# Kernel optimization log

Hardware: AMD Instinct MI355X
Metric: run time of the kernel (lower is better)

The kernel has to match this reference:

```python
import jax, jax.numpy as jnp
import numpy as np

N = 8192          # num nodes
E = 262144        # num edges
F_IN = 512        # dataset.num_features
HID = 256         # hidden_dim
C = 16            # dataset.num_classes
ALPHA = 1.0
GAMMA = 1.0
EPS = 0.4
LN_EPS = 1e-5


def setup_inputs() -> dict:
    key = jax.random.key(0)
    ks = jax.random.split(key, 16)
    x = jax.random.normal(ks[0], (N, F_IN), dtype=jnp.float32)
    edge_index = jax.random.randint(ks[1], (2, E), 0, N, dtype=jnp.int64)
    def lin(k, fan_in, fan_out):
        s = 1.0 / np.sqrt(fan_in)
        return jax.random.uniform(k, (fan_in, fan_out), jnp.float32, -s, s)
    return {
        "x": x,
        "edge_index": edge_index,
        "W0": lin(ks[2], F_IN, HID), "b0": jnp.zeros((HID,), jnp.float32),
        "ln0_g": jnp.ones((HID,), jnp.float32), "ln0_b": jnp.zeros((HID,), jnp.float32),
        "W1": lin(ks[3], HID, HID), "b1": jnp.zeros((HID,), jnp.float32),
        "ln1_g": jnp.ones((HID,), jnp.float32), "ln1_b": jnp.zeros((HID,), jnp.float32),
        "W2": lin(ks[4], HID, C), "b2": jnp.zeros((C,), jnp.float32),
    }


def _layernorm(h, g, b):
    mu = jnp.mean(h, axis=-1, keepdims=True)
    var = jnp.var(h, axis=-1, keepdims=True)
    return (h - mu) * jax.lax.rsqrt(var + LN_EPS) * g + b


def _hpf_weight_matrix(edge_index, n, dtype):
    # to_dense_adj with parallel-edge accumulation
    A = jnp.zeros((n, n), dtype).at[edge_index[0], edge_index[1]].add(jnp.asarray(1.0, dtype))
    eye = jnp.eye(n, dtype=dtype)
    A = GAMMA * A + ALPHA * eye
    # D^{-1/2} A D^{-1/2} as fused row/col scaling (same math as the two diag matmuls)
    dinv = jax.lax.rsqrt(jnp.sum(A, axis=1))
    A_hat = dinv[:, None] * A * dinv[None, :]
    # (eps - 1) I + (I - A_hat) == eps*I - A_hat ; keep only positive entries (edge extraction)
    U = EPS * eye - A_hat
    return jnp.where(U > 0, U, jnp.asarray(0.0, dtype))


def reference(x, edge_index, W0, b0, ln0_g, ln0_b, W1, b1, ln1_g, ln1_b, W2, b2):
    Wmat = _hpf_weight_matrix(edge_index, x.shape[0], x.dtype)
    # GCNConv(normalize=False): h' = scatter_{src->tgt}(w * (h@W)[src]) + bias == Wmat^T @ (h@W) + b
    def gcn(h, W, b):
        return Wmat.T @ (h @ W) + b
    h = gcn(x, W0, b0)
    h = _layernorm(jax.nn.relu(h), ln0_g, ln0_b)   # dropout p=0.0 -> identity
    h = gcn(h, W1, b1)
    h = _layernorm(jax.nn.relu(h), ln1_g, ln1_b)
    embedding = gcn(h, W2, b2)
    return embedding, jax.nn.log_softmax(embedding, axis=1)
```

## Files before the change

kernel.cpp:

```cpp
#include <hip/hip_runtime.h>

#define NN 8192
#define NE 262144
#define FIN 512
#define HIDN 256
#define NC 16

typedef __attribute__((ext_vector_type(8))) short bf16x8;
typedef __attribute__((ext_vector_type(4))) short bf16x4;
typedef __attribute__((ext_vector_type(4))) float f32x4;

static __device__ __forceinline__ unsigned short f2bf(float f) {
    union { float f; unsigned u; } v; v.f = f;
    unsigned r = v.u + 0x7FFFu + ((v.u >> 16) & 1u);
    return (unsigned short)(r >> 16);
}

template<int K, int N>
static __device__ __forceinline__ void pack_w(const float* __restrict__ W,
                                              unsigned short* __restrict__ Wp, int f) {
    constexpr int KC = K / 32;
    int lane = f & 63;
    int g = f >> 6;
    int kc = g % KC;
    int nt = g / KC;
    int n = nt * 16 + (lane & 15);
    int kbase = kc * 32 + (lane >> 4) * 8;
    bf16x8 v;
#pragma unroll
    for (int j = 0; j < 8; ++j) v[j] = (short)f2bf(W[(kbase + j) * N + n]);
    *(bf16x8*)&Wp[f * 8] = v;
}

__global__ __launch_bounds__(512) void work_kernel(
    const int* __restrict__ ei,
    const float* __restrict__ W0, const float* __restrict__ W1, const float* __restrict__ W2,
    int* __restrict__ cnt,
    unsigned short* __restrict__ Wp0, unsigned short* __restrict__ Wp1,
    unsigned short* __restrict__ Wp2)
{
    const int tid = threadIdx.x, bid = blockIdx.x;
    if (bid < 207) {
        const int p = bid * 512 + tid;
#pragma unroll
        for (int i = 0; i < 2; ++i) {
            int c = p + i * 105984;
            if (c < NE / 2) {
                int2 s2 = *(const int2*)&ei[c * 2];
                int2 t2 = *(const int2*)&ei[NE + c * 2];
                atomicAdd(&cnt[s2.x], 1);
                atomicAdd(&cnt[s2.y], 1);
                if (s2.x == t2.x) atomicAdd(&cnt[NN + s2.x], 1);
                if (s2.y == t2.y) atomicAdd(&cnt[NN + s2.y], 1);
            }
        }
    } else {
        int gp = (bid - 207) * 512 + tid;
        if (gp < 16384)       pack_w<512, 256>(W0, Wp0, gp);
        else if (gp < 24576)  pack_w<256, 256>(W1, Wp1, gp - 16384);
        else                  pack_w<256, 16 >(W2, Wp2, gp - 24576);
    }
}

static __device__ __forceinline__ void ln_epilogue(
    const f32x4 acc[4], const float* __restrict__ bias, const float* __restrict__ gam,
    const float* __restrict__ bet, const float wdr[4],
    int half, int wq, int quad, int l16,
    unsigned short* sH, float red[][8])
{
    float bv[4], gv[4], btv[4];
#pragma unroll
    for (int nt = 0; nt < 4; ++nt) {
        int col = wq * 64 + nt * 16 + l16;
        bv[nt] = bias[col]; gv[nt] = gam[col]; btv[nt] = bet[col];
    }
    float vv[4][4], s[4], ss[4];
#pragma unroll
    for (int reg = 0; reg < 4; ++reg) {
        float ps = 0.f, pss = 0.f;
#pragma unroll
        for (int nt = 0; nt < 4; ++nt) {
            float v = fmaxf(fmaf(wdr[reg], acc[nt][reg], bv[nt]), 0.f);
            vv[nt][reg] = v;
            ps += v; pss += v * v;
        }
        s[reg] = ps; ss[reg] = pss;
    }
#pragma unroll
    for (int off = 1; off < 16; off <<= 1)
#pragma unroll
        for (int reg = 0; reg < 4; ++reg) {
            s[reg]  += __shfl_xor(s[reg],  off, 64);
            ss[reg] += __shfl_xor(ss[reg], off, 64);
        }
    __syncthreads();
    if (l16 == 0) {
#pragma unroll
        for (int reg = 0; reg < 4; ++reg) {
            int rl = half * 16 + quad * 4 + reg;
            red[rl][wq * 2]     = s[reg];
            red[rl][wq * 2 + 1] = ss[reg];
        }
    }
    __syncthreads();
#pragma unroll
    for (int reg = 0; reg < 4; ++reg) {
        int rl = half * 16 + quad * 4 + reg;
        float ts  = red[rl][0] + red[rl][2] + red[rl][4] + red[rl][6];
        float tss = red[rl][1] + red[rl][3] + red[rl][5] + red[rl][7];
        float mu  = ts * (1.0f / 256.0f);
        float var = tss * (1.0f / 256.0f) - mu * mu;
        float rs  = rsqrtf(var + 1e-5f);
#pragma unroll
        for (int nt = 0; nt < 4; ++nt) {
            float o = (vv[nt][reg] - mu) * rs * gv[nt] + btv[nt];
            sH[rl * 264 + wq * 64 + nt * 16 + l16] = f2bf(o);
        }
    }
    __syncthreads();
}

__global__ __launch_bounds__(512) void mega_kernel(
    const float* __restrict__ x,
    const unsigned short* __restrict__ Wp0, const unsigned short* __restrict__ Wp1,
    const unsigned short* __restrict__ Wp2,
    const float* __restrict__ b0, const float* __restrict__ g0, const float* __restrict__ be0,
    const float* __restrict__ b1, const float* __restrict__ g1, const float* __restrict__ be1,
    const float* __restrict__ b2, const int* __restrict__ cnt,
    float* __restrict__ out)
{
    __shared__ unsigned short sX[32 * 136];
    __shared__ unsigned short sH[32 * 264];
    __shared__ float red[32][8];
    __shared__ float swd[32];

    const int tid  = threadIdx.x;
    const int lane = tid & 63, wave = tid >> 6;
    const int quad = lane >> 4, l16 = lane & 15;
    const int half = wave >> 2, wq = wave & 3;
    const int row0 = blockIdx.x * 32;

    if (tid < 32) {
        int base = cnt[2 * NN];
        int d  = cnt[row0 + tid]      - base;
        int sl = cnt[NN + row0 + tid] - base;
        float u = 0.4f - (1.0f + (float)sl) / (1.0f + (float)d);
        swd[tid] = u > 0.0f ? u : 0.0f;
    }
    __syncthreads();
    float wdr[4];
#pragma unroll
    for (int reg = 0; reg < 4; ++reg) wdr[reg] = swd[half * 16 + quad * 4 + reg];

    const bf16x8* Wp0v = (const bf16x8*)Wp0;
    const bf16x8* Wp1v = (const bf16x8*)Wp1;
    const bf16x8* Wp2v = (const bf16x8*)Wp2;
    const float4* x4 = (const float4*)x;

    f32x4 acc[4];
#pragma unroll
    for (int nt = 0; nt < 4; ++nt) acc[nt] = (f32x4){0.f, 0.f, 0.f, 0.f};

    for (int kb = 0; kb < 4; ++kb) {
#pragma unroll
        for (int i = 0; i < 2; ++i) {
            int f = tid + i * 512;
            int r = f >> 5, c4 = f & 31;
            float4 v = x4[(row0 + r) * 128 + kb * 32 + c4];
            bf16x4 h;
            h[0] = (short)f2bf(v.x); h[1] = (short)f2bf(v.y);
            h[2] = (short)f2bf(v.z); h[3] = (short)f2bf(v.w);
            *(bf16x4*)&sX[r * 136 + c4 * 4] = h;
        }
        __syncthreads();
#pragma unroll
        for (int kc = 0; kc < 4; ++kc) {
            bf16x8 a = *(const bf16x8*)&sX[(half * 16 + l16) * 136 + kc * 32 + quad * 8];
#pragma unroll
            for (int nt = 0; nt < 4; ++nt) {
                bf16x8 b = Wp0v[((wq * 4 + nt) * 16 + kb * 4 + kc) * 64 + lane];
                acc[nt] = __builtin_amdgcn_mfma_f32_16x16x32_bf16(a, b, acc[nt], 0, 0, 0);
            }
        }
        __syncthreads();
    }
    ln_epilogue(acc, b0, g0, be0, wdr, half, wq, quad, l16, sH, red);

    f32x4 acc1[4];
#pragma unroll
    for (int nt = 0; nt < 4; ++nt) acc1[nt] = (f32x4){0.f, 0.f, 0.f, 0.f};
#pragma unroll
    for (int kc = 0; kc < 8; ++kc) {
        bf16x8 a = *(const bf16x8*)&sH[(half * 16 + l16) * 264 + kc * 32 + quad * 8];
#pragma unroll
        for (int nt = 0; nt < 4; ++nt) {
            bf16x8 b = Wp1v[((wq * 4 + nt) * 8 + kc) * 64 + lane];
            acc1[nt] = __builtin_amdgcn_mfma_f32_16x16x32_bf16(a, b, acc1[nt], 0, 0, 0);
        }
    }
    ln_epilogue(acc1, b1, g1, be1, wdr, half, wq, quad, l16, sH, red);

    if (wq == 0) {
        f32x4 acch = (f32x4){0.f, 0.f, 0.f, 0.f};
#pragma unroll
        for (int kc = 0; kc < 8; ++kc) {
            bf16x8 a = *(const bf16x8*)&sH[(half * 16 + l16) * 264 + kc * 32 + quad * 8];
            bf16x8 b = Wp2v[kc * 64 + lane];
            acch = __builtin_amdgcn_mfma_f32_16x16x32_bf16(a, b, acch, 0, 0, 0);
        }
        float bb = b2[l16];
#pragma unroll
        for (int reg = 0; reg < 4; ++reg) {
            int row = row0 + half * 16 + quad * 4 + reg;
            float v = fmaf(wdr[reg], acch[reg], bb);
            float m = v;
#pragma unroll
            for (int off = 8; off >= 1; off >>= 1) m = fmaxf(m, __shfl_xor(m, off, 64));
            float e = __expf(v - m);
            float se = e;
#pragma unroll
            for (int off = 8; off >= 1; off >>= 1) se += __shfl_xor(se, off, 64);
            float lsm = (v - m) - __logf(se);
            out[row * 16 + l16] = v;
            out[NN * 16 + row * 16 + l16] = lsm;
        }
    }
}

extern "C" void kernel_launch(void* const* d_in, const int* in_sizes, int n_in,
                              void* d_out, int out_size, void* d_ws, size_t ws_size,
                              hipStream_t stream) {
    const float* x  = (const float*)d_in[0];
    const int*   ei = (const int*)d_in[1];
    const float* W0 = (const float*)d_in[2];
    const float* b0 = (const float*)d_in[3];
    const float* g0 = (const float*)d_in[4];
    const float* be0 = (const float*)d_in[5];
    const float* W1 = (const float*)d_in[6];
    const float* b1 = (const float*)d_in[7];
    const float* g1 = (const float*)d_in[8];
    const float* be1 = (const float*)d_in[9];
    const float* W2 = (const float*)d_in[10];
    const float* b2 = (const float*)d_in[11];
    float* out = (float*)d_out;

    char* ws = (char*)d_ws;
    int*            cnt = (int*)ws;
    unsigned short* Wp0 = (unsigned short*)(ws + 68 * 1024);
    unsigned short* Wp1 = (unsigned short*)(ws + 324 * 1024);
    unsigned short* Wp2 = (unsigned short*)(ws + 452 * 1024);

    work_kernel<<<256, 512, 0, stream>>>(ei, W0, W1, W2, cnt, Wp0, Wp1, Wp2);
    mega_kernel<<<NN / 32, 512, 0, stream>>>(x, Wp0, Wp1, Wp2,
                                             b0, g0, be0, b1, g1, be1, b2, cnt, out);
}
```

Baseline: 109.1 us.

## Fuse degree counting, weight packing and MLP into one cooperative kernel

Merges the preprocessing kernel (edge degree/self-loop atomics and bf16 weight packing) and the main per-row GEMM/LayerNorm kernel into a single cooperative launch of 256 blocks. A software grid barrier on a counter in the workspace separates the phases, and the x tile is loaded into LDS before the barrier so that load overlaps the wait. The goal is to remove the second kernel launch and its gap. The cost is a spin barrier, a larger LDS footprint, and reliance on the counter base from earlier runs. The old two-kernel path is kept as a fallback if the cooperative launch fails.

```diff
diff --git a/kernel.cpp b/kernel.cpp
--- a/kernel.cpp
+++ b/kernel.cpp
@@ -32,6 +32,206 @@
     *(bf16x8*)&Wp[f * 8] = v;
 }
 
+static __device__ __forceinline__ void ln_epilogue(
+    const f32x4 acc[4], const float* __restrict__ bias, const float* __restrict__ gam,
+    const float* __restrict__ bet, const float wdr[4],
+    int half, int wq, int quad, int l16,
+    unsigned short* sH, float red[][8])
+{
+    float bv[4], gv[4], btv[4];
+#pragma unroll
+    for (int nt = 0; nt < 4; ++nt) {
+        int col = wq * 64 + nt * 16 + l16;
+        bv[nt] = bias[col]; gv[nt] = gam[col]; btv[nt] = bet[col];
+    }
+    float vv[4][4], s[4], ss[4];
+#pragma unroll
+    for (int reg = 0; reg < 4; ++reg) {
+        float ps = 0.f, pss = 0.f;
+#pragma unroll
+        for (int nt = 0; nt < 4; ++nt) {
+            float v = fmaxf(fmaf(wdr[reg], acc[nt][reg], bv[nt]), 0.f);
+            vv[nt][reg] = v;
+            ps += v; pss += v * v;
+        }
+        s[reg] = ps; ss[reg] = pss;
+    }
+#pragma unroll
+    for (int off = 1; off < 16; off <<= 1)
+#pragma unroll
+        for (int reg = 0; reg < 4; ++reg) {
+            s[reg]  += __shfl_xor(s[reg],  off, 64);
+            ss[reg] += __shfl_xor(ss[reg], off, 64);
+        }
+    __syncthreads();
+    if (l16 == 0) {
+#pragma unroll
+        for (int reg = 0; reg < 4; ++reg) {
+            int rl = half * 16 + quad * 4 + reg;
+            red[rl][wq * 2]     = s[reg];
+            red[rl][wq * 2 + 1] = ss[reg];
+        }
+    }
+    __syncthreads();
+#pragma unroll
+    for (int reg = 0; reg < 4; ++reg) {
+        int rl = half * 16 + quad * 4 + reg;
+        float ts  = red[rl][0] + red[rl][2] + red[rl][4] + red[rl][6];
+        float tss = red[rl][1] + red[rl][3] + red[rl][5] + red[rl][7];
+        float mu  = ts * (1.0f / 256.0f);
+        float var = tss * (1.0f / 256.0f) - mu * mu;
+        float rs  = rsqrtf(var + 1e-5f);
+#pragma unroll
+        for (int nt = 0; nt < 4; ++nt) {
+            float o = (vv[nt][reg] - mu) * rs * gv[nt] + btv[nt];
+            sH[rl * 264 + wq * 64 + nt * 16 + l16] = f2bf(o);
+        }
+    }
+    __syncthreads();
+}
+
+__global__ __launch_bounds__(512) void fused_kernel(
+    const float* __restrict__ x, const int* __restrict__ ei,
+    const float* __restrict__ W0, const float* __restrict__ W1, const float* __restrict__ W2,
+    const float* __restrict__ b0, const float* __restrict__ g0, const float* __restrict__ be0,
+    const float* __restrict__ b1, const float* __restrict__ g1, const float* __restrict__ be1,
+    const float* __restrict__ b2,
+    int* __restrict__ cnt,
+    unsigned short* __restrict__ Wp0, unsigned short* __restrict__ Wp1,
+    unsigned short* __restrict__ Wp2,
+    float* __restrict__ out)
+{
+    __shared__ unsigned short sX[32 * 520];
+    __shared__ unsigned short sH[32 * 264];
+    __shared__ float red[32][8];
+    __shared__ float swd[32];
+
+    const int tid  = threadIdx.x, bid = blockIdx.x;
+    const int lane = tid & 63, wave = tid >> 6;
+    const int quad = lane >> 4, l16 = lane & 15;
+    const int half = wave >> 2, wq = wave & 3;
+    const int row0 = bid * 32;
+
+    if (bid < 207) {
+        const int p = bid * 512 + tid;
+#pragma unroll
+        for (int i = 0; i < 2; ++i) {
+            int c = p + i * 105984;
+            if (c < NE / 2) {
+                int2 s2 = *(const int2*)&ei[c * 2];
+                int2 t2 = *(const int2*)&ei[NE + c * 2];
+                atomicAdd(&cnt[s2.x], 1);
+                atomicAdd(&cnt[s2.y], 1);
+                if (s2.x == t2.x) atomicAdd(&cnt[NN + s2.x], 1);
+                if (s2.y == t2.y) atomicAdd(&cnt[NN + s2.y], 1);
+            }
+        }
+    } else {
+        int gp = (bid - 207) * 512 + tid;
+        if (gp < 16384)       pack_w<512, 256>(W0, Wp0, gp);
+        else if (gp < 24576)  pack_w<256, 256>(W1, Wp1, gp - 16384);
+        else                  pack_w<256, 16 >(W2, Wp2, gp - 24576);
+    }
+
+    const float4* x4 = (const float4*)x;
+#pragma unroll
+    for (int i = 0; i < 4; ++i) {
+        int idx = i * 1024 + tid * 2;
+        float4 v0 = x4[row0 * 128 + idx];
+        float4 v1 = x4[row0 * 128 + idx + 1];
+        int r = idx >> 7, c4 = idx & 127;
+        bf16x8 h;
+        h[0] = (short)f2bf(v0.x); h[1] = (short)f2bf(v0.y);
+        h[2] = (short)f2bf(v0.z); h[3] = (short)f2bf(v0.w);
+        h[4] = (short)f2bf(v1.x); h[5] = (short)f2bf(v1.y);
+        h[6] = (short)f2bf(v1.z); h[7] = (short)f2bf(v1.w);
+        *(bf16x8*)&sX[r * 520 + c4 * 4] = h;
+    }
+
+    __threadfence();
+    __syncthreads();
+    if (tid == 0) {
+        int base = cnt[2 * NN];
+        int* bar = &cnt[2 * NN + 1];
+        __hip_atomic_fetch_add(bar, 1, __ATOMIC_RELAXED, __HIP_MEMORY_SCOPE_AGENT);
+        while ((unsigned)(__hip_atomic_load(bar, __ATOMIC_RELAXED,
+                                            __HIP_MEMORY_SCOPE_AGENT) - base) < 256u)
+            __builtin_amdgcn_s_sleep(1);
+    }
+    __syncthreads();
+    __threadfence();
+
+    if (tid < 32) {
+        int base = cnt[2 * NN];
+        int d  = cnt[row0 + tid]      - base;
+        int sl = cnt[NN + row0 + tid] - base;
+        float u = 0.4f - (1.0f + (float)sl) / (1.0f + (float)d);
+        swd[tid] = u > 0.0f ? u : 0.0f;
+    }
+    __syncthreads();
+    float wdr[4];
+#pragma unroll
+    for (int reg = 0; reg < 4; ++reg) wdr[reg] = swd[half * 16 + quad * 4 + reg];
+
+    const bf16x8* Wp0v = (const bf16x8*)Wp0;
+    const bf16x8* Wp1v = (const bf16x8*)Wp1;
+    const bf16x8* Wp2v = (const bf16x8*)Wp2;
+
+    f32x4 acc[4];
+#pragma unroll
+    for (int nt = 0; nt < 4; ++nt) acc[nt] = (f32x4){0.f, 0.f, 0.f, 0.f};
+#pragma unroll
+    for (int kc = 0; kc < 16; ++kc) {
+        bf16x8 a = *(const bf16x8*)&sX[(half * 16 + l16) * 520 + kc * 32 + quad * 8];
+#pragma unroll
+        for (int nt = 0; nt < 4; ++nt) {
+            bf16x8 b = Wp0v[((wq * 4 + nt) * 16 + kc) * 64 + lane];
+            acc[nt] = __builtin_amdgcn_mfma_f32_16x16x32_bf16(a, b, acc[nt], 0, 0, 0);
+        }
+    }
+    ln_epilogue(acc, b0, g0, be0, wdr, half, wq, quad, l16, sH, red);
+
+    f32x4 acc1[4];
+#pragma unroll
+    for (int nt = 0; nt < 4; ++nt) acc1[nt] = (f32x4){0.f, 0.f, 0.f, 0.f};
+#pragma unroll
+    for (int kc = 0; kc < 8; ++kc) {
+        bf16x8 a = *(const bf16x8*)&sH[(half * 16 + l16) * 264 + kc * 32 + quad * 8];
+#pragma unroll
+        for (int nt = 0; nt < 4; ++nt) {
+            bf16x8 b = Wp1v[((wq * 4 + nt) * 8 + kc) * 64 + lane];
+            acc1[nt] = __builtin_amdgcn_mfma_f32_16x16x32_bf16(a, b, acc1[nt], 0, 0, 0);
+        }
+    }
+    ln_epilogue(acc1, b1, g1, be1, wdr, half, wq, quad, l16, sH, red);
+
+    if (wq == 0) {
+        f32x4 acch = (f32x4){0.f, 0.f, 0.f, 0.f};
+#pragma unroll
+        for (int kc = 0; kc < 8; ++kc) {
+            bf16x8 a = *(const bf16x8*)&sH[(half * 16 + l16) * 264 + kc * 32 + quad * 8];
+            bf16x8 b = Wp2v[kc * 64 + lane];
+            acch = __builtin_amdgcn_mfma_f32_16x16x32_bf16(a, b, acch, 0, 0, 0);
+        }
+        float bb = b2[l16];
+#pragma unroll
+        for (int reg = 0; reg < 4; ++reg) {
+            int row = row0 + half * 16 + quad * 4 + reg;
+            float v = fmaf(wdr[reg], acch[reg], bb);
+            float m = v;
+#pragma unroll
+            for (int off = 8; off >= 1; off >>= 1) m = fmaxf(m, __shfl_xor(m, off, 64));
+            float e = __expf(v - m);
+            float se = e;
+#pragma unroll
+            for (int off = 8; off >= 1; off >>= 1) se += __shfl_xor(se, off, 64);
+            float lsm = (v - m) - __logf(se);
+            out[row * 16 + l16] = v;
+            out[NN * 16 + row * 16 + l16] = lsm;
+        }
+    }
+}
+
 __global__ __launch_bounds__(512) void work_kernel(
     const int* __restrict__ ei,
     const float* __restrict__ W0, const float* __restrict__ W1, const float* __restrict__ W2,
@@ -60,64 +260,6 @@
         else if (gp < 24576)  pack_w<256, 256>(W1, Wp1, gp - 16384);
         else                  pack_w<256, 16 >(W2, Wp2, gp - 24576);
     }
-}
-
-static __device__ __forceinline__ void ln_epilogue(
-    const f32x4 acc[4], const float* __restrict__ bias, const float* __restrict__ gam,
-    const float* __restrict__ bet, const float wdr[4],
-    int half, int wq, int quad, int l16,
-    unsigned short* sH, float red[][8])
-{
-    float bv[4], gv[4], btv[4];
-#pragma unroll
-    for (int nt = 0; nt < 4; ++nt) {
-        int col = wq * 64 + nt * 16 + l16;
-        bv[nt] = bias[col]; gv[nt] = gam[col]; btv[nt] = bet[col];
-    }
-    float vv[4][4], s[4], ss[4];
-#pragma unroll
-    for (int reg = 0; reg < 4; ++reg) {
-        float ps = 0.f, pss = 0.f;
-#pragma unroll
-        for (int nt = 0; nt < 4; ++nt) {
-            float v = fmaxf(fmaf(wdr[reg], acc[nt][reg], bv[nt]), 0.f);
-            vv[nt][reg] = v;
-            ps += v; pss += v * v;
-        }
-        s[reg] = ps; ss[reg] = pss;
-    }
-#pragma unroll
-    for (int off = 1; off < 16; off <<= 1)
-#pragma unroll
-        for (int reg = 0; reg < 4; ++reg) {
-            s[reg]  += __shfl_xor(s[reg],  off, 64);
-            ss[reg] += __shfl_xor(ss[reg], off, 64);
-        }
-    __syncthreads();
-    if (l16 == 0) {
-#pragma unroll
-        for (int reg = 0; reg < 4; ++reg) {
-            int rl = half * 16 + quad * 4 + reg;
-            red[rl][wq * 2]     = s[reg];
-            red[rl][wq * 2 + 1] = ss[reg];
-        }
-    }
-    __syncthreads();
-#pragma unroll
-    for (int reg = 0; reg < 4; ++reg) {
-        int rl = half * 16 + quad * 4 + reg;
-        float ts  = red[rl][0] + red[rl][2] + red[rl][4] + red[rl][6];
-        float tss = red[rl][1] + red[rl][3] + red[rl][5] + red[rl][7];
-        float mu  = ts * (1.0f / 256.0f);
-        float var = tss * (1.0f / 256.0f) - mu * mu;
-        float rs  = rsqrtf(var + 1e-5f);
-#pragma unroll
-        for (int nt = 0; nt < 4; ++nt) {
-            float o = (vv[nt][reg] - mu) * rs * gv[nt] + btv[nt];
-            sH[rl * 264 + wq * 64 + nt * 16 + l16] = f2bf(o);
-        }
-    }
-    __syncthreads();
 }
 
 __global__ __launch_bounds__(512) void mega_kernel(
@@ -250,7 +392,15 @@
     unsigned short* Wp1 = (unsigned short*)(ws + 324 * 1024);
     unsigned short* Wp2 = (unsigned short*)(ws + 452 * 1024);
 
-    work_kernel<<<256, 512, 0, stream>>>(ei, W0, W1, W2, cnt, Wp0, Wp1, Wp2);
-    mega_kernel<<<NN / 32, 512, 0, stream>>>(x, Wp0, Wp1, Wp2,
-                                             b0, g0, be0, b1, g1, be1, b2, cnt, out);
-}
+    void* args[] = { (void*)&x, (void*)&ei, (void*)&W0, (void*)&W1, (void*)&W2,
+                     (void*)&b0, (void*)&g0, (void*)&be0,
+                     (void*)&b1, (void*)&g1, (void*)&be1, (void*)&b2,
+                     (void*)&cnt, (void*)&Wp0, (void*)&Wp1, (void*)&Wp2, (void*)&out };
+    hipError_t err = hipLaunchCooperativeKernel((const void*)fused_kernel,
+                                                dim3(256), dim3(512), args, 0, stream);
+    if (err != hipSuccess) {
+        work_kernel<<<256, 512, 0, stream>>>(ei, W0, W1, W2, cnt, Wp0, Wp1, Wp2);
+        mega_kernel<<<NN / 32, 512, 0, stream>>>(x, Wp0, Wp1, Wp2,
+                                                 b0, g0, be0, b1, g1, be1, b2, cnt, out);
+    }
+}
```

New measurement: 232.0 us. +112.6%, slower.

## Use 16-row blocks with full-K x staging and 8-way column split

Applied to the files above, without the earlier changes.

Shrinks each block of the fused MLP kernel from 32 to 16 rows, doubling the grid to 512 blocks, and assigns each of the 8 waves 32 output columns instead of splitting rows into halves. The whole 16x512 x tile is loaded up front in a single pass and converted to bf16 into shared memory, replacing the 4-step K loop that synchronised twice per step. The goal is more parallelism across CUs and fewer barriers. In exchange, each packed weight fragment is reused over only 16 rows, so weight traffic from L2 doubles.

```diff
diff --git a/kernel.cpp b/kernel.cpp
--- a/kernel.cpp
+++ b/kernel.cpp
@@ -63,23 +63,23 @@
 }
 
 static __device__ __forceinline__ void ln_epilogue(
-    const f32x4 acc[4], const float* __restrict__ bias, const float* __restrict__ gam,
+    const f32x4 acc[2], const float* __restrict__ bias, const float* __restrict__ gam,
     const float* __restrict__ bet, const float wdr[4],
-    int half, int wq, int quad, int l16,
-    unsigned short* sH, float red[][8])
+    int w, int quad, int l16,
+    unsigned short* sH, float red[][16])
 {
-    float bv[4], gv[4], btv[4];
-#pragma unroll
-    for (int nt = 0; nt < 4; ++nt) {
-        int col = wq * 64 + nt * 16 + l16;
+    float bv[2], gv[2], btv[2];
+#pragma unroll
+    for (int nt = 0; nt < 2; ++nt) {
+        int col = w * 32 + nt * 16 + l16;
         bv[nt] = bias[col]; gv[nt] = gam[col]; btv[nt] = bet[col];
     }
-    float vv[4][4], s[4], ss[4];
+    float vv[2][4], s[4], ss[4];
 #pragma unroll
     for (int reg = 0; reg < 4; ++reg) {
         float ps = 0.f, pss = 0.f;
 #pragma unroll
-        for (int nt = 0; nt < 4; ++nt) {
+        for (int nt = 0; nt < 2; ++nt) {
             float v = fmaxf(fmaf(wdr[reg], acc[nt][reg], bv[nt]), 0.f);
             vv[nt][reg] = v;
             ps += v; pss += v * v;
@@ -97,24 +97,25 @@
     if (l16 == 0) {
 #pragma unroll
         for (int reg = 0; reg < 4; ++reg) {
-            int rl = half * 16 + quad * 4 + reg;
-            red[rl][wq * 2]     = s[reg];
-            red[rl][wq * 2 + 1] = ss[reg];
+            int rl = quad * 4 + reg;
+            red[rl][w * 2]     = s[reg];
+            red[rl][w * 2 + 1] = ss[reg];
         }
     }
     __syncthreads();
 #pragma unroll
     for (int reg = 0; reg < 4; ++reg) {
-        int rl = half * 16 + quad * 4 + reg;
-        float ts  = red[rl][0] + red[rl][2] + red[rl][4] + red[rl][6];
-        float tss = red[rl][1] + red[rl][3] + red[rl][5] + red[rl][7];
+        int rl = quad * 4 + reg;
+        float ts = 0.f, tss = 0.f;
+#pragma unroll
+        for (int i = 0; i < 8; ++i) { ts += red[rl][2 * i]; tss += red[rl][2 * i + 1]; }
         float mu  = ts * (1.0f / 256.0f);
         float var = tss * (1.0f / 256.0f) - mu * mu;
         float rs  = rsqrtf(var + 1e-5f);
 #pragma unroll
-        for (int nt = 0; nt < 4; ++nt) {
+        for (int nt = 0; nt < 2; ++nt) {
             float o = (vv[nt][reg] - mu) * rs * gv[nt] + btv[nt];
-            sH[rl * 264 + wq * 64 + nt * 16 + l16] = f2bf(o);
+            sH[rl * 264 + w * 32 + nt * 16 + l16] = f2bf(o);
         }
     }
     __syncthreads();
@@ -129,89 +130,97 @@
     const float* __restrict__ b2, const int* __restrict__ cnt,
     float* __restrict__ out)
 {
-    __shared__ unsigned short sX[32 * 136];
-    __shared__ unsigned short sH[32 * 264];
-    __shared__ float red[32][8];
-    __shared__ float swd[32];
+    __shared__ unsigned short sX[16 * 520];
+    __shared__ unsigned short sH[16 * 264];
+    __shared__ float red[16][16];
+    __shared__ float swd[16];
 
     const int tid  = threadIdx.x;
-    const int lane = tid & 63, wave = tid >> 6;
+    const int lane = tid & 63, w = tid >> 6;
     const int quad = lane >> 4, l16 = lane & 15;
-    const int half = wave >> 2, wq = wave & 3;
-    const int row0 = blockIdx.x * 32;
-
-    if (tid < 32) {
+    const int row0 = blockIdx.x * 16;
+
+    const float4* x4 = (const float4*)x;
+    const int idx0 = tid * 2;
+    float4 v0 = x4[row0 * 128 + idx0];
+    float4 v1 = x4[row0 * 128 + idx0 + 1];
+    float4 v2 = x4[row0 * 128 + 1024 + idx0];
+    float4 v3 = x4[row0 * 128 + 1024 + idx0 + 1];
+
+    if (tid < 16) {
         int base = cnt[2 * NN];
         int d  = cnt[row0 + tid]      - base;
         int sl = cnt[NN + row0 + tid] - base;
         float u = 0.4f - (1.0f + (float)sl) / (1.0f + (float)d);
         swd[tid] = u > 0.0f ? u : 0.0f;
     }
-    __syncthreads();
+
+    {
+        int r = idx0 >> 7, c4 = idx0 & 127;
+        bf16x8 h;
+        h[0] = (short)f2bf(v0.x); h[1] = (short)f2bf(v0.y);
+        h[2] = (short)f2bf(v0.z); h[3] = (short)f2bf(v0.w);
+        h[4] = (short)f2bf(v1.x); h[5] = (short)f2bf(v1.y);
+        h[6] = (short)f2bf(v1.z); h[7] = (short)f2bf(v1.w);
+        *(bf16x8*)&sX[r * 520 + c4 * 4] = h;
+        int idx1 = idx0 + 1024;
+        r = idx1 >> 7; c4 = idx1 & 127;
+        h[0] = (short)f2bf(v2.x); h[1] = (short)f2bf(v2.y);
+        h[2] = (short)f2bf(v2.z); h[3] = (short)f2bf(v2.w);
+        h[4] = (short)f2bf(v3.x); h[5] = (short)f2bf(v3.y);
+        h[6] = (short)f2bf(v3.z); h[7] = (short)f2bf(v3.w);
+        *(bf16x8*)&sX[r * 520 + c4 * 4] = h;
+    }
+    __syncthreads();
+
     float wdr[4];
 #pragma unroll
-    for (int reg = 0; reg < 4; ++reg) wdr[reg] = swd[half * 16 + quad * 4 + reg];
+    for (int reg = 0; reg < 4; ++reg) wdr[reg] = swd[quad * 4 + reg];
 
     const bf16x8* Wp0v = (const bf16x8*)Wp0;
     const bf16x8* Wp1v = (const bf16x8*)Wp1;
     const bf16x8* Wp2v = (const bf16x8*)Wp2;
-    const float4* x4 = (const float4*)x;
-
-    f32x4 acc[4];
-#pragma unroll
-    for (int nt = 0; nt < 4; ++nt) acc[nt] = (f32x4){0.f, 0.f, 0.f, 0.f};
-
-    for (int kb = 0; kb < 4; ++kb) {
-#pragma unroll
-        for (int i = 0; i < 2; ++i) {
-            int f = tid + i * 512;
-            int r = f >> 5, c4 = f & 31;
-            float4 v = x4[(row0 + r) * 128 + kb * 32 + c4];
-            bf16x4 h;
-            h[0] = (short)f2bf(v.x); h[1] = (short)f2bf(v.y);
-            h[2] = (short)f2bf(v.z); h[3] = (short)f2bf(v.w);
-            *(bf16x4*)&sX[r * 136 + c4 * 4] = h;
-        }
-        __syncthreads();
-#pragma unroll
-        for (int kc = 0; kc < 4; ++kc) {
-            bf16x8 a = *(const bf16x8*)&sX[(half * 16 + l16) * 136 + kc * 32 + quad * 8];
-#pragma unroll
-            for (int nt = 0; nt < 4; ++nt) {
-                bf16x8 b = Wp0v[((wq * 4 + nt) * 16 + kb * 4 + kc) * 64 + lane];
-                acc[nt] = __builtin_amdgcn_mfma_f32_16x16x32_bf16(a, b, acc[nt], 0, 0, 0);
-            }
-        }
-        __syncthreads();
-    }
-    ln_epilogue(acc, b0, g0, be0, wdr, half, wq, quad, l16, sH, red);
-
-    f32x4 acc1[4];
-#pragma unroll
-    for (int nt = 0; nt < 4; ++nt) acc1[nt] = (f32x4){0.f, 0.f, 0.f, 0.f};
+
+    f32x4 acc[2];
+#pragma unroll
+    for (int nt = 0; nt < 2; ++nt) acc[nt] = (f32x4){0.f, 0.f, 0.f, 0.f};
+#pragma unroll
+    for (int kc = 0; kc < 16; ++kc) {
+        bf16x8 a = *(const bf16x8*)&sX[l16 * 520 + kc * 32 + quad * 8];
+#pragma unroll
+        for (int nt = 0; nt < 2; ++nt) {
+            bf16x8 b = Wp0v[((w * 2 + nt) * 16 + kc) * 64 + lane];
+            acc[nt] = __builtin_amdgcn_mfma_f32_16x16x32_bf16(a, b, acc[nt], 0, 0, 0);
+        }
+    }
+    ln_epilogue(acc, b0, g0, be0, wdr, w, quad, l16, sH, red);
+
+    f32x4 acc1[2];
+#pragma unroll
+    for (int nt = 0; nt < 2; ++nt) acc1[nt] = (f32x4){0.f, 0.f, 0.f, 0.f};
 #pragma unroll
     for (int kc = 0; kc < 8; ++kc) {
-        bf16x8 a = *(const bf16x8*)&sH[(half * 16 + l16) * 264 + kc * 32 + quad * 8];
-#pragma unroll
-        for (int nt = 0; nt < 4; ++nt) {
-            bf16x8 b = Wp1v[((wq * 4 + nt) * 8 + kc) * 64 + lane];
+        bf16x8 a = *(const bf16x8*)&sH[l16 * 264 + kc * 32 + quad * 8];
+#pragma unroll
+        for (int nt = 0; nt < 2; ++nt) {
+            bf16x8 b = Wp1v[((w * 2 + nt) * 8 + kc) * 64 + lane];
             acc1[nt] = __builtin_amdgcn_mfma_f32_16x16x32_bf16(a, b, acc1[nt], 0, 0, 0);
         }
     }
-    ln_epilogue(acc1, b1, g1, be1, wdr, half, wq, quad, l16, sH, red);
-
-    if (wq == 0) {
+    ln_epilogue(acc1, b1, g1, be1, wdr, w, quad, l16, sH, red);
+
+    if (w == 0) {
         f32x4 acch = (f32x4){0.f, 0.f, 0.f, 0.f};
 #pragma unroll
         for (int kc = 0; kc < 8; ++kc) {
-            bf16x8 a = *(const bf16x8*)&sH[(half * 16 + l16) * 264 + kc * 32 + quad * 8];
+            bf16x8 a = *(const bf16x8*)&sH[l16 * 264 + kc * 32 + quad * 8];
             bf16x8 b = Wp2v[kc * 64 + lane];
             acch = __builtin_amdgcn_mfma_f32_16x16x32_bf16(a, b, acch, 0, 0, 0);
         }
         float bb = b2[l16];
 #pragma unroll
         for (int reg = 0; reg < 4; ++reg) {
-            int row = row0 + half * 16 + quad * 4 + reg;
+            int row = row0 + quad * 4 + reg;
             float v = fmaf(wdr[reg], acch[reg], bb);
             float m = v;
 #pragma unroll
@@ -251,6 +260,6 @@
     unsigned short* Wp2 = (unsigned short*)(ws + 452 * 1024);
 
     work_kernel<<<256, 512, 0, stream>>>(ei, W0, W1, W2, cnt, Wp0, Wp1, Wp2);
-    mega_kernel<<<NN / 32, 512, 0, stream>>>(x, Wp0, Wp1, Wp2,
+    mega_kernel<<<NN / 16, 512, 0, stream>>>(x, Wp0, Wp1, Wp2,
                                              b0, g0, be0, b1, g1, be1, b2, cnt, out);
 }
```

Result: no change. 109.0 us (-0.1%).
